# Kernel tuning notes

Hardware: AMD Instinct MI355X
Metric: run time of the kernel (lower is better)

## Reference

```python
import jax, jax.numpy as jnp
import numpy as np

NUM_CLASSES = 80
NUM_ANCHORS = 3
IN_H, IN_W = 608, 608
GRID_H, GRID_W = 76, 76
BATCH = 16
# anchors selected by anchor_mask [0,1,2] out of the 9 COCO anchors
MASKED_ANCHORS = np.array([[10.0, 13.0], [16.0, 30.0], [33.0, 23.0]], dtype=np.float32)


def setup_inputs() -> dict:
    key = jax.random.key(0)
    x = jax.random.normal(key, (BATCH, NUM_ANCHORS * (5 + NUM_CLASSES), GRID_H, GRID_W), dtype=jnp.float32)
    anchors = jnp.asarray(MASKED_ANCHORS)
    return {"x": x, "anchors": anchors}


def reference(x, anchors):
    """YOLOv3 detection-layer forward (decode path of Yolo.__cal_bounding_box).

    x: [N, A*(5+C), H, W] raw conv output; anchors: [A, 2] (w, h) in pixels.
    Returns decoded predictions [N, A*H*W, 5+C] with normalized xywh boxes,
    objectness and class probabilities.
    """
    N, _, H, W = x.shape
    A, C = NUM_ANCHORS, NUM_CLASSES
    x = x.reshape(N, A, 5 + C, H, W)  # [N, A, 5+C, H, W]

    px = jax.nn.sigmoid(x[:, :, 0])            # [N, A, H, W]
    py = jax.nn.sigmoid(x[:, :, 1])
    pw = x[:, :, 2]
    ph = x[:, :, 3]
    conf = jax.nn.sigmoid(x[:, :, 4])          # [N, A, H, W]
    prob = jax.nn.sigmoid(x[:, :, 5:])         # [N, A, C, H, W]

    gy, gx = jnp.meshgrid(jnp.arange(H, dtype=x.dtype), jnp.arange(W, dtype=x.dtype), indexing="ij")
    # grid-offset decode, normalized to [0, 1] (matches __cal_bounding_box)
    bx = (px + gx) / W
    by = (py + gy) / H
    aw = anchors[:, 0].reshape(1, A, 1, 1)
    ah = anchors[:, 1].reshape(1, A, 1, 1)
    bw = jnp.exp(pw) * aw / IN_W
    bh = jnp.exp(ph) * ah / IN_H

    bbox = jnp.stack([bx, by, bw, bh, conf], axis=-1)      # [N, A, H, W, 5]
    prob = jnp.transpose(prob, (0, 1, 3, 4, 2))            # [N, A, H, W, C]
    out = jnp.concatenate([bbox, prob], axis=-1)           # [N, A, H, W, 5+C]
    return out.reshape(N, A * H * W, 5 + C)
```

## Files before the change

### kernel.cpp

```cpp
#include <hip/hip_runtime.h>
#include <math.h>


#define NCH     85
#define SPATIAL 5776
#define GWID    76
#define TS      128
#define TSP     129
#define NTILES  46

__device__ __forceinline__ float fast_sigmoid(float v) {
    return __builtin_amdgcn_rcpf(1.0f + __expf(-v));
}

__global__ __launch_bounds__(256) void yolo_decode(
    const float* __restrict__ x,
    const float* __restrict__ anchors,
    float* __restrict__ out)
{
    __shared__ float tile[NCH * TSP];

    const int na  = blockIdx.y;
    const int a   = na % 3;
    const int s0  = blockIdx.x * TS;
    const int rem = min(TS, SPATIAL - s0);
    const int t   = threadIdx.x;

    const float* in_base = x + (size_t)na * NCH * SPATIAL + s0;

    if (rem == TS) {
        for (int g = t; g < NCH * (TS / 4); g += 256) {
            const int c  = g >> 5;
            const int s4 = (g & 31) << 2;
            const float4 v = *reinterpret_cast<const float4*>(in_base + c * SPATIAL + s4);
            float* dst = &tile[c * TSP + s4];
            dst[0] = v.x; dst[1] = v.y; dst[2] = v.z; dst[3] = v.w;
        }
    } else {
        for (int g = t; g < NCH * rem; g += 256) {
            const int c = g / rem;
            const int s = g - c * rem;
            tile[c * TSP + s] = in_base[c * SPATIAL + s];
        }
    }
    __syncthreads();

    const float aw = anchors[a * 2 + 0] * (1.0f / 608.0f);
    const float ah = anchors[a * 2 + 1] * (1.0f / 608.0f);

    float* out_base = out + ((size_t)na * SPATIAL + s0) * NCH;
    const int nv4 = (NCH * rem) >> 2;

    for (int v = t; v < nv4; v += 256) {
        const int fb = v << 2;
        float4 o;
        float* op = &o.x;
        #pragma unroll
        for (int j = 0; j < 4; ++j) {
            const int f = fb + j;
            const int s = f / NCH;
            const int c = f - s * NCH;
            const float val = tile[c * TSP + s];
            const int sg = s0 + s;
            float r;
            if (c == 0) {
                r = (fast_sigmoid(val) + (float)(sg % GWID)) * (1.0f / GWID);
            } else if (c == 1) {
                r = (fast_sigmoid(val) + (float)(sg / GWID)) * (1.0f / GWID);
            } else if (c == 2) {
                r = __expf(val) * aw;
            } else if (c == 3) {
                r = __expf(val) * ah;
            } else {
                r = fast_sigmoid(val);
            }
            op[j] = r;
        }
        *reinterpret_cast<float4*>(out_base + fb) = o;
    }
}

extern "C" void kernel_launch(void* const* d_in, const int* in_sizes, int n_in,
                              void* d_out, int out_size, void* d_ws, size_t ws_size,
                              hipStream_t stream) {
    const float* x       = (const float*)d_in[0];
    const float* anchors = (const float*)d_in[1];
    float* out           = (float*)d_out;

    dim3 grid(NTILES, 48);
    yolo_decode<<<grid, 256, 0, stream>>>(x, anchors, out);
}
```

Baseline: 198.3 us.

## Apply activations during load and store output-major tile with vector copies

Moves the per-element sigmoid/exp decode from the write phase into the load phase, where each thread's channel is uniform across its float4. The shared tile is now stored in output order (spatial-major, channel-minor), so the write phase becomes a plain float4 copy with no divisions by 85 or branch divergence. The tile size is halved to 64 spatial positions, which doubles the block count and lowers LDS use per block. The transposed scalar stores into LDS with stride 85 may cause bank conflicts, and the tail tile assumes the remainder is 16.

```diff
diff --git a/kernel.cpp b/kernel.cpp
--- a/kernel.cpp
+++ b/kernel.cpp
@@ -5,9 +5,8 @@
 #define NCH     85
 #define SPATIAL 5776
 #define GWID    76
-#define TS      128
-#define TSP     129
-#define NTILES  46
+#define TS      64
+#define NTILES  91
 
 __device__ __forceinline__ float fast_sigmoid(float v) {
     return __builtin_amdgcn_rcpf(1.0f + __expf(-v));
@@ -18,65 +17,73 @@
     const float* __restrict__ anchors,
     float* __restrict__ out)
 {
-    __shared__ float tile[NCH * TSP];
+    __shared__ __align__(16) float tile[NCH * TS];
 
     const int na  = blockIdx.y;
     const int a   = na % 3;
     const int s0  = blockIdx.x * TS;
-    const int rem = min(TS, SPATIAL - s0);
+    const int rem = (s0 + TS <= SPATIAL) ? TS : (SPATIAL - s0);
     const int t   = threadIdx.x;
-
-    const float* in_base = x + (size_t)na * NCH * SPATIAL + s0;
-
-    if (rem == TS) {
-        for (int g = t; g < NCH * (TS / 4); g += 256) {
-            const int c  = g >> 5;
-            const int s4 = (g & 31) << 2;
-            const float4 v = *reinterpret_cast<const float4*>(in_base + c * SPATIAL + s4);
-            float* dst = &tile[c * TSP + s4];
-            dst[0] = v.x; dst[1] = v.y; dst[2] = v.z; dst[3] = v.w;
-        }
-    } else {
-        for (int g = t; g < NCH * rem; g += 256) {
-            const int c = g / rem;
-            const int s = g - c * rem;
-            tile[c * TSP + s] = in_base[c * SPATIAL + s];
-        }
-    }
-    __syncthreads();
 
     const float aw = anchors[a * 2 + 0] * (1.0f / 608.0f);
     const float ah = anchors[a * 2 + 1] * (1.0f / 608.0f);
 
+    const float* in_base = x + (size_t)na * NCH * SPATIAL + s0;
+
+    #define PROCESS(cc, sl4)                                                     \
+        do {                                                                     \
+            const int c  = (cc);                                                 \
+            const int sl = (sl4);                                                \
+            const float4 v = *reinterpret_cast<const float4*>(                   \
+                in_base + c * SPATIAL + sl);                                     \
+            float vv[4] = {v.x, v.y, v.z, v.w};                                  \
+            if (c >= 4) {                       \
+                _Pragma("unroll")                                                \
+                for (int jj = 0; jj < 4; ++jj)                                   \
+                    tile[(sl + jj) * NCH + c] = fast_sigmoid(vv[jj]);            \
+            } else if (c == 0) {                                                 \
+                _Pragma("unroll")                                                \
+                for (int jj = 0; jj < 4; ++jj) {                                 \
+                    const int sg = s0 + sl + jj;                                 \
+                    tile[(sl + jj) * NCH + c] =                                  \
+                        (fast_sigmoid(vv[jj]) + (float)(sg % GWID)) *            \
+                        (1.0f / GWID);                                           \
+                }                                                                \
+            } else if (c == 1) {                                                 \
+                _Pragma("unroll")                                                \
+                for (int jj = 0; jj < 4; ++jj) {                                 \
+                    const int sg = s0 + sl + jj;                                 \
+                    tile[(sl + jj) * NCH + c] =                                  \
+                        (fast_sigmoid(vv[jj]) + (float)(sg / GWID)) *            \
+                        (1.0f / GWID);                                           \
+                }                                                                \
+            } else if (c == 2) {                                                 \
+                _Pragma("unroll")                                                \
+                for (int jj = 0; jj < 4; ++jj)                                   \
+                    tile[(sl + jj) * NCH + c] = __expf(vv[jj]) * aw;             \
+            } else {                                                 \
+                _Pragma("unroll")                                                \
+                for (int jj = 0; jj < 4; ++jj)                                   \
+                    tile[(sl + jj) * NCH + c] = __expf(vv[jj]) * ah;             \
+            }                                                                    \
+        } while (0)
+
+    if (rem == TS) {
+        for (int idx = t; idx < NCH * (TS / 4); idx += 256)
+            PROCESS(idx >> 4, (idx & 15) << 2);
+    } else {
+        for (int idx = t; idx < NCH * 4; idx += 256)
+            PROCESS(idx >> 2, (idx & 3) << 2);
+    }
+    #undef PROCESS
+
+    __syncthreads();
+
     float* out_base = out + ((size_t)na * SPATIAL + s0) * NCH;
     const int nv4 = (NCH * rem) >> 2;
-
     for (int v = t; v < nv4; v += 256) {
-        const int fb = v << 2;
-        float4 o;
-        float* op = &o.x;
-        #pragma unroll
-        for (int j = 0; j < 4; ++j) {
-            const int f = fb + j;
-            const int s = f / NCH;
-            const int c = f - s * NCH;
-            const float val = tile[c * TSP + s];
-            const int sg = s0 + s;
-            float r;
-            if (c == 0) {
-                r = (fast_sigmoid(val) + (float)(sg % GWID)) * (1.0f / GWID);
-            } else if (c == 1) {
-                r = (fast_sigmoid(val) + (float)(sg / GWID)) * (1.0f / GWID);
-            } else if (c == 2) {
-                r = __expf(val) * aw;
-            } else if (c == 3) {
-                r = __expf(val) * ah;
-            } else {
-                r = fast_sigmoid(val);
-            }
-            op[j] = r;
-        }
-        *reinterpret_cast<float4*>(out_base + fb) = o;
+        const float4 o = *reinterpret_cast<const float4*>(&tile[v << 2]);
+        *reinterpret_cast<float4*>(out_base + (v << 2)) = o;
     }
 }
 
```

New measurement: 170.9 us. 13.8% less time.

## Compute activations on load and store transposed tile for float4 copy-out

Applied to the files above, without the earlier changes.

Moves the sigmoid/exp math into the load phase so each value is computed once with its channel known up front, and writes results into shared memory already in output order (spatial-major, 85 floats per point). The store phase becomes a plain float4 copy from shared memory to global with no per-element divide/modulo or branching. The tile shrinks to 64 positions, doubling the block count, and all loads are issued up front per thread. The trade-off is that the shared-memory writes are now strided by 85 per position, which may cause bank conflicts.

```diff
diff --git a/kernel.cpp b/kernel.cpp
--- a/kernel.cpp
+++ b/kernel.cpp
@@ -5,12 +5,44 @@
 #define NCH     85
 #define SPATIAL 5776
 #define GWID    76
-#define TS      128
-#define TSP     129
-#define NTILES  46
+#define TS      64
+#define NTILES  91
 
 __device__ __forceinline__ float fast_sigmoid(float v) {
     return __builtin_amdgcn_rcpf(1.0f + __expf(-v));
+}
+
+__device__ __forceinline__ void process4(float* __restrict__ tile,
+                                         int c, int sl, int s0,
+                                         float4 v, float aw, float ah) {
+    float vv[4] = {v.x, v.y, v.z, v.w};
+    if (c >= 4) {
+        #pragma unroll
+        for (int jj = 0; jj < 4; ++jj)
+            tile[(sl + jj) * NCH + c] = fast_sigmoid(vv[jj]);
+    } else if (c == 0) {
+        #pragma unroll
+        for (int jj = 0; jj < 4; ++jj) {
+            const int sg = s0 + sl + jj;
+            tile[(sl + jj) * NCH + c] =
+                (fast_sigmoid(vv[jj]) + (float)(sg % GWID)) * (1.0f / GWID);
+        }
+    } else if (c == 1) {
+        #pragma unroll
+        for (int jj = 0; jj < 4; ++jj) {
+            const int sg = s0 + sl + jj;
+            tile[(sl + jj) * NCH + c] =
+                (fast_sigmoid(vv[jj]) + (float)(sg / GWID)) * (1.0f / GWID);
+        }
+    } else if (c == 2) {
+        #pragma unroll
+        for (int jj = 0; jj < 4; ++jj)
+            tile[(sl + jj) * NCH + c] = __expf(vv[jj]) * aw;
+    } else {
+        #pragma unroll
+        for (int jj = 0; jj < 4; ++jj)
+            tile[(sl + jj) * NCH + c] = __expf(vv[jj]) * ah;
+    }
 }
 
 __global__ __launch_bounds__(256) void yolo_decode(
@@ -18,65 +50,76 @@
     const float* __restrict__ anchors,
     float* __restrict__ out)
 {
-    __shared__ float tile[NCH * TSP];
+    __shared__ __align__(16) float tile[NCH * TS];
 
     const int na  = blockIdx.y;
     const int a   = na % 3;
     const int s0  = blockIdx.x * TS;
-    const int rem = min(TS, SPATIAL - s0);
     const int t   = threadIdx.x;
-
-    const float* in_base = x + (size_t)na * NCH * SPATIAL + s0;
-
-    if (rem == TS) {
-        for (int g = t; g < NCH * (TS / 4); g += 256) {
-            const int c  = g >> 5;
-            const int s4 = (g & 31) << 2;
-            const float4 v = *reinterpret_cast<const float4*>(in_base + c * SPATIAL + s4);
-            float* dst = &tile[c * TSP + s4];
-            dst[0] = v.x; dst[1] = v.y; dst[2] = v.z; dst[3] = v.w;
-        }
-    } else {
-        for (int g = t; g < NCH * rem; g += 256) {
-            const int c = g / rem;
-            const int s = g - c * rem;
-            tile[c * TSP + s] = in_base[c * SPATIAL + s];
-        }
-    }
-    __syncthreads();
 
     const float aw = anchors[a * 2 + 0] * (1.0f / 608.0f);
     const float ah = anchors[a * 2 + 1] * (1.0f / 608.0f);
 
+    const float* in_base = x + (size_t)na * NCH * SPATIAL + s0;
     float* out_base = out + ((size_t)na * SPATIAL + s0) * NCH;
-    const int nv4 = (NCH * rem) >> 2;
 
-    for (int v = t; v < nv4; v += 256) {
-        const int fb = v << 2;
-        float4 o;
-        float* op = &o.x;
-        #pragma unroll
-        for (int j = 0; j < 4; ++j) {
-            const int f = fb + j;
-            const int s = f / NCH;
-            const int c = f - s * NCH;
-            const float val = tile[c * TSP + s];
-            const int sg = s0 + s;
-            float r;
-            if (c == 0) {
-                r = (fast_sigmoid(val) + (float)(sg % GWID)) * (1.0f / GWID);
-            } else if (c == 1) {
-                r = (fast_sigmoid(val) + (float)(sg / GWID)) * (1.0f / GWID);
-            } else if (c == 2) {
-                r = __expf(val) * aw;
-            } else if (c == 3) {
-                r = __expf(val) * ah;
-            } else {
-                r = fast_sigmoid(val);
-            }
-            op[j] = r;
+    if (s0 + TS <= SPATIAL) {
+        const int sl    = (t & 15) << 2;
+        const int cbase = t >> 4;
+        const bool extra = (t < 80);
+
+        const float* p = in_base + cbase * SPATIAL + sl;
+        float4 v0 = *reinterpret_cast<const float4*>(p);
+        float4 v1 = *reinterpret_cast<const float4*>(p + 16 * SPATIAL);
+        float4 v2 = *reinterpret_cast<const float4*>(p + 32 * SPATIAL);
+        float4 v3 = *reinterpret_cast<const float4*>(p + 48 * SPATIAL);
+        float4 v4 = *reinterpret_cast<const float4*>(p + 64 * SPATIAL);
+        float4 vt;
+        int ct = 80 + cbase;
+        if (extra)
+            vt = *reinterpret_cast<const float4*>(in_base + ct * SPATIAL + sl);
+
+        process4(tile, cbase +  0, sl, s0, v0, aw, ah);
+        process4(tile, cbase + 16, sl, s0, v1, aw, ah);
+        process4(tile, cbase + 32, sl, s0, v2, aw, ah);
+        process4(tile, cbase + 48, sl, s0, v3, aw, ah);
+        process4(tile, cbase + 64, sl, s0, v4, aw, ah);
+        if (extra)
+            process4(tile, ct, sl, s0, vt, aw, ah);
+
+        __syncthreads();
+
+        const int fb = t << 2;
+        float4 o0 = *reinterpret_cast<const float4*>(&tile[fb]);
+        float4 o1 = *reinterpret_cast<const float4*>(&tile[fb + 1024]);
+        float4 o2 = *reinterpret_cast<const float4*>(&tile[fb + 2048]);
+        float4 o3 = *reinterpret_cast<const float4*>(&tile[fb + 3072]);
+        float4 o4 = *reinterpret_cast<const float4*>(&tile[fb + 4096]);
+        *reinterpret_cast<float4*>(out_base + fb)        = o0;
+        *reinterpret_cast<float4*>(out_base + fb + 1024) = o1;
+        *reinterpret_cast<float4*>(out_base + fb + 2048) = o2;
+        *reinterpret_cast<float4*>(out_base + fb + 3072) = o3;
+        *reinterpret_cast<float4*>(out_base + fb + 4096) = o4;
+        if (extra) {
+            const int fbt = 5120 + (t << 2);
+            float4 ot = *reinterpret_cast<const float4*>(&tile[fbt]);
+            *reinterpret_cast<float4*>(out_base + fbt) = ot;
         }
-        *reinterpret_cast<float4*>(out_base + fb) = o;
+    } else {
+        const int rem = SPATIAL - s0;
+        for (int idx = t; idx < NCH * (rem / 4); idx += 256) {
+            const int c  = idx / (rem / 4);
+            const int sl = (idx - c * (rem / 4)) << 2;
+            const float4 v = *reinterpret_cast<const float4*>(
+                in_base + c * SPATIAL + sl);
+            process4(tile, c, sl, s0, v, aw, ah);
+        }
+        __syncthreads();
+        const int nv4 = (NCH * rem) >> 2;
+        for (int v = t; v < nv4; v += 256) {
+            const float4 o = *reinterpret_cast<const float4*>(&tile[v << 2]);
+            *reinterpret_cast<float4*>(out_base + (v << 2)) = o;
+        }
     }
 }
 
```

After: 168.7 us. -14.9%, faster.

## Use two-row tiles, compute during load, and store transposed tile with float4 copies

Applied to the files above, without the earlier changes.

Tiles now span two full grid rows (152 spatial positions), so the 38 tiles divide the spatial extent exactly and the ragged tail path goes away. The decode math moves into the load phase, and results are written into shared memory already in output order, so the store phase is a plain float4 copy. All loads are issued up front in an unrolled sequence with 512 threads per block. The cost is strided shared-memory writes (stride 85) in the scatter, which may cause bank conflicts, plus higher register use and larger blocks.

```diff
diff --git a/kernel.cpp b/kernel.cpp
--- a/kernel.cpp
+++ b/kernel.cpp
@@ -4,79 +4,101 @@
 
 #define NCH     85
 #define SPATIAL 5776
-#define GWID    76
-#define TS      128
-#define TSP     129
-#define NTILES  46
+#define GW      76
+#define TS      152
+#define NTILES  38
+#define NF4     (NCH * TS / 4)
+#define EXTRA_T (NF4 - 512 * 6)
 
 __device__ __forceinline__ float fast_sigmoid(float v) {
     return __builtin_amdgcn_rcpf(1.0f + __expf(-v));
 }
 
-__global__ __launch_bounds__(256) void yolo_decode(
+__device__ __forceinline__ void scatter4(float* __restrict__ tile,
+                                         int c, int k, int j2,
+                                         float4 v, float aw, float ah) {
+    float vv[4] = {v.x, v.y, v.z, v.w};
+    #pragma unroll
+    for (int jj = 0; jj < 4; ++jj) {
+        const int pos = 4 * k + jj;
+        float r;
+        if (c == 0) {
+            const int gx = (pos < GW) ? pos : pos - GW;
+            r = (fast_sigmoid(vv[jj]) + (float)gx) * (1.0f / GW);
+        } else if (c == 1) {
+            const int gy = j2 + ((pos >= GW) ? 1 : 0);
+            r = (fast_sigmoid(vv[jj]) + (float)gy) * (1.0f / GW);
+        } else if (c == 2) {
+            r = __expf(vv[jj]) * aw;
+        } else if (c == 3) {
+            r = __expf(vv[jj]) * ah;
+        } else {
+            r = fast_sigmoid(vv[jj]);
+        }
+        tile[pos * NCH + c] = r;
+    }
+}
+
+__global__ __launch_bounds__(512) void yolo_decode(
     const float* __restrict__ x,
     const float* __restrict__ anchors,
     float* __restrict__ out)
 {
-    __shared__ float tile[NCH * TSP];
+    __shared__ __align__(16) float tile[NCH * TS];
 
-    const int na  = blockIdx.y;
-    const int a   = na % 3;
-    const int s0  = blockIdx.x * TS;
-    const int rem = min(TS, SPATIAL - s0);
-    const int t   = threadIdx.x;
+    const int j  = blockIdx.x;
+    const int na = blockIdx.y;
+    const int a  = na % 3;
+    const int s0 = j * TS;
+    const int t  = threadIdx.x;
+    const int j2 = 2 * j;
+
+    const float aw = anchors[2 * a]     * (1.0f / 608.0f);
+    const float ah = anchors[2 * a + 1] * (1.0f / 608.0f);
 
     const float* in_base = x + (size_t)na * NCH * SPATIAL + s0;
+    float* out_base = out + ((size_t)na * SPATIAL + s0) * NCH;
 
-    if (rem == TS) {
-        for (int g = t; g < NCH * (TS / 4); g += 256) {
-            const int c  = g >> 5;
-            const int s4 = (g & 31) << 2;
-            const float4 v = *reinterpret_cast<const float4*>(in_base + c * SPATIAL + s4);
-            float* dst = &tile[c * TSP + s4];
-            dst[0] = v.x; dst[1] = v.y; dst[2] = v.z; dst[3] = v.w;
-        }
-    } else {
-        for (int g = t; g < NCH * rem; g += 256) {
-            const int c = g / rem;
-            const int s = g - c * rem;
-            tile[c * TSP + s] = in_base[c * SPATIAL + s];
-        }
+    int c[7], k[7];
+    #pragma unroll
+    for (int i = 0; i < 7; ++i) {
+        const int m = t + 512 * i;
+        c[i] = m / 38;
+        k[i] = m - 38 * c[i];
     }
+    const bool extra = (t < EXTRA_T);
+
+    float4 v0 = *reinterpret_cast<const float4*>(in_base + c[0] * SPATIAL + 4 * k[0]);
+    float4 v1 = *reinterpret_cast<const float4*>(in_base + c[1] * SPATIAL + 4 * k[1]);
+    float4 v2 = *reinterpret_cast<const float4*>(in_base + c[2] * SPATIAL + 4 * k[2]);
+    float4 v3 = *reinterpret_cast<const float4*>(in_base + c[3] * SPATIAL + 4 * k[3]);
+    float4 v4 = *reinterpret_cast<const float4*>(in_base + c[4] * SPATIAL + 4 * k[4]);
+    float4 v5 = *reinterpret_cast<const float4*>(in_base + c[5] * SPATIAL + 4 * k[5]);
+    float4 v6;
+    if (extra)
+        v6 = *reinterpret_cast<const float4*>(in_base + c[6] * SPATIAL + 4 * k[6]);
+
+    scatter4(tile, c[0], k[0], j2, v0, aw, ah);
+    scatter4(tile, c[1], k[1], j2, v1, aw, ah);
+    scatter4(tile, c[2], k[2], j2, v2, aw, ah);
+    scatter4(tile, c[3], k[3], j2, v3, aw, ah);
+    scatter4(tile, c[4], k[4], j2, v4, aw, ah);
+    scatter4(tile, c[5], k[5], j2, v5, aw, ah);
+    if (extra)
+        scatter4(tile, c[6], k[6], j2, v6, aw, ah);
+
     __syncthreads();
 
-    const float aw = anchors[a * 2 + 0] * (1.0f / 608.0f);
-    const float ah = anchors[a * 2 + 1] * (1.0f / 608.0f);
-
-    float* out_base = out + ((size_t)na * SPATIAL + s0) * NCH;
-    const int nv4 = (NCH * rem) >> 2;
-
-    for (int v = t; v < nv4; v += 256) {
-        const int fb = v << 2;
-        float4 o;
-        float* op = &o.x;
-        #pragma unroll
-        for (int j = 0; j < 4; ++j) {
-            const int f = fb + j;
-            const int s = f / NCH;
-            const int c = f - s * NCH;
-            const float val = tile[c * TSP + s];
-            const int sg = s0 + s;
-            float r;
-            if (c == 0) {
-                r = (fast_sigmoid(val) + (float)(sg % GWID)) * (1.0f / GWID);
-            } else if (c == 1) {
-                r = (fast_sigmoid(val) + (float)(sg / GWID)) * (1.0f / GWID);
-            } else if (c == 2) {
-                r = __expf(val) * aw;
-            } else if (c == 3) {
-                r = __expf(val) * ah;
-            } else {
-                r = fast_sigmoid(val);
-            }
-            op[j] = r;
-        }
-        *reinterpret_cast<float4*>(out_base + fb) = o;
+    #pragma unroll
+    for (int i = 0; i < 6; ++i) {
+        const int m = t + 512 * i;
+        const float4 o = *reinterpret_cast<const float4*>(&tile[4 * m]);
+        *reinterpret_cast<float4*>(out_base + 4 * m) = o;
+    }
+    if (extra) {
+        const int m = t + 512 * 6;
+        const float4 o = *reinterpret_cast<const float4*>(&tile[4 * m]);
+        *reinterpret_cast<float4*>(out_base + 4 * m) = o;
     }
 }
 
@@ -88,5 +110,5 @@
     float* out           = (float*)d_out;
 
     dim3 grid(NTILES, 48);
-    yolo_decode<<<grid, 256, 0, stream>>>(x, anchors, out);
+    yolo_decode<<<grid, 512, 0, stream>>>(x, anchors, out);
 }
```

Result: faster. 169.5 us (-14.5%).
